# Kernel tuning notes

Measured on AMD Instinct MI355X. Metric: run time of the kernel, lower is better.

## Reference

```python
import jax, jax.numpy as jnp
import numpy as np
import math

NUM_HEADS = 16
HEAVY_RATIO = 0.1
RECENT_RATIO = 0.1
ROPE_THETA = 10000.0


def setup_inputs() -> dict:
    key = jax.random.key(0)
    ks = jax.random.split(key, 5)
    b, s, h = 1, 2048, 2048
    return {
        "hidden_states": jax.random.normal(ks[0], (b, s, h), dtype=jnp.float32),
        "Wq": jax.random.normal(ks[1], (h, h), dtype=jnp.float32) * 0.02,
        "Wk": jax.random.normal(ks[2], (h, h), dtype=jnp.float32) * 0.02,
        "Wv": jax.random.normal(ks[3], (h, h), dtype=jnp.float32) * 0.02,
        "Wo": jax.random.normal(ks[4], (h, h), dtype=jnp.float32) * 0.02,
    }


def _rotate_half(x):
    d = x.shape[-1]
    return jnp.concatenate([-x[..., d // 2:], x[..., : d // 2]], axis=-1)


def _rope(q, k, seq_len, head_dim, dtype):
    # LLaMA rotary embedding: inv_freq over even dims, emb = [freqs, freqs]
    inv_freq = 1.0 / (ROPE_THETA ** (jnp.arange(0, head_dim, 2, dtype=jnp.float32) / head_dim))
    pos = jnp.arange(seq_len, dtype=jnp.float32)
    freqs = pos[:, None] * inv_freq[None, :]            # [s, d/2]
    emb = jnp.concatenate([freqs, freqs], axis=-1)       # [s, d]
    cos = jnp.cos(emb).astype(dtype)[None, None]         # [1,1,s,d]
    sin = jnp.sin(emb).astype(dtype)[None, None]
    q = q * cos + _rotate_half(q) * sin
    k = k * cos + _rotate_half(k) * sin
    return q, k


def reference(hidden_states, Wq, Wk, Wv, Wo):
    b, s, hidden = hidden_states.shape
    H = NUM_HEADS
    d = hidden // H

    def proj(W):  # nn.Linear(x) = x @ W.T, then split heads -> [b,H,s,d]
        return (hidden_states @ W.T).reshape(b, s, H, d).transpose(0, 2, 1, 3)

    q, k, v = proj(Wq), proj(Wk), proj(Wv)
    q, k = _rope(q, k, s, d, hidden_states.dtype)

    scores = jnp.einsum("bhqd,bhkd->bhqk", q, k) / math.sqrt(d)  # [b,H,s,s]
    neg = jnp.finfo(scores.dtype).min
    i = jnp.arange(s)[:, None]
    j = jnp.arange(s)[None, :]
    causal = jnp.where(j <= i, jnp.array(0.0, scores.dtype), neg)
    scores = jnp.maximum(scores + causal, neg)

    heavy_budget = int(HEAVY_RATIO * s)
    recent_budget = int(RECENT_RATIO * s)

    # first softmax (fp32), accumulate column importances
    tmp_attn = jax.nn.softmax(scores.astype(jnp.float32), axis=-1).astype(scores.dtype)
    tmp_sum = jnp.sum(tmp_attn, axis=-2)                 # [b,H,s]
    _, topk_idx = jax.lax.top_k(tmp_sum, heavy_budget)   # [b,H,heavy]
    heavy_mask = jnp.any(topk_idx[..., :, None] == jnp.arange(s)[None, None, None, :], axis=-2)  # [b,H,s]

    # recent band: tril(diag=recent) & triu(diag=-recent)  <=>  |i-j| <= recent
    band = jnp.abs(i - j) <= recent_budget               # [s,s]
    mask = heavy_mask[:, :, None, :] | band[None, None]

    scores = jnp.where(mask, scores, neg)
    probs = jax.nn.softmax(scores.astype(jnp.float32), axis=-1).astype(q.dtype)
    attn = jnp.einsum("bhqk,bhkd->bhqd", probs, v)
    attn = attn.transpose(0, 2, 1, 3).reshape(b, s, hidden)
    return attn @ Wo.T
```

## Files before the change

### kernel.cpp

```cpp
#include <hip/hip_runtime.h>
#include <hip/hip_bf16.h>
#include <stdint.h>

#define SEQ   2048
#define HIDN  2048
#define NHEAD 16
#define HDIM  128
#define HEAVY 204
#define RECENT 204

typedef __attribute__((ext_vector_type(4))) float f32x4;
typedef __attribute__((ext_vector_type(8))) short bf16x8;
typedef unsigned short u16;
typedef unsigned int   u32;

static __device__ __forceinline__ u16 f2bf(float f){
  union { float f; u32 u; } v; v.f = f;
  u32 r = (v.u + 0x7FFFu + ((v.u >> 16) & 1u)) >> 16;
  return (u16)r;
}
static __device__ __forceinline__ float bf2f(u16 u){
  union { u32 u; float f; } v; v.u = ((u32)u) << 16;
  return v.f;
}

static __device__ __forceinline__ void gload16(const void* g, void* l){
  __builtin_amdgcn_global_load_lds((const __attribute__((address_space(1))) u32*)g,
                                   (__attribute__((address_space(3))) u32*)l, 16, 0, 0);
}

#define WAITVM(N) asm volatile("s_waitcnt vmcnt(" #N ")" ::: "memory")
#define BARRAW    __builtin_amdgcn_s_barrier()
#define PRIO1     __builtin_amdgcn_s_setprio(1)
#define PRIO0     __builtin_amdgcn_s_setprio(0)

static __device__ __forceinline__ void stage_tile(const u16* __restrict__ base, size_t stride,
                                                  int row0, u16* __restrict__ lds, int tid){
  const int wbase = tid & ~63;
#pragma unroll
  for (int it = 0; it < 4; ++it){
    int m = it * 256 + tid;
    int row = m >> 4, cp = m & 15;
    gload16(base + (size_t)(row0 + row) * stride + ((cp ^ (row & 7)) * 8),
            lds + (it * 256 + wbase) * 8);
  }
}

static __device__ __forceinline__ void stageK512(const u16* __restrict__ base, size_t stride,
                                                 int row0, u16* __restrict__ lds, int tid){
#pragma unroll
  for (int it = 0; it < 2; ++it){
    int m = it * 512 + tid;
    int row = m >> 4, cp = m & 15;
    gload16(base + (size_t)(row0 + row) * stride + ((cp ^ (row & 7)) * 8),
            lds + (it * 512 + (tid & ~63)) * 8);
  }
}
static __device__ __forceinline__ void stageV512(const u16* __restrict__ base, size_t stride,
                                                 int c0, u16* __restrict__ lds, int tid){
#pragma unroll
  for (int it = 0; it < 2; ++it){
    int m = it * 512 + tid;
    int row = m >> 3, cp = m & 7;
    gload16(base + (size_t)row * stride + c0 + ((cp ^ (row & 7)) * 8),
            lds + (it * 512 + (tid & ~63)) * 8);
  }
}

__global__ void k_prep(const float* __restrict__ A0, const float* __restrict__ A1,
                       const float* __restrict__ A2, const float* __restrict__ A3,
                       const float* __restrict__ A4, u16* __restrict__ out,
                       float* __restrict__ cosT, float* __restrict__ sinT,
                       float* __restrict__ colsum){
  int b = blockIdx.x, tid = threadIdx.x;
  if (b < 20480){
    int id = b * 256 + tid;
    int sel = id >> 20, off = (id & 1048575) * 4;
    const float* src = sel == 0 ? A0 : sel == 1 ? A1 : sel == 2 ? A2 : sel == 3 ? A3 : A4;
    float4 v = *(const float4*)(src + off);
    ushort4 o;
    o.x = f2bf(v.x); o.y = f2bf(v.y); o.z = f2bf(v.z); o.w = f2bf(v.w);
    *(ushort4*)(out + (size_t)sel * 4194304 + off) = o;
  } else if (b < 20992){
    int i = (b - 20480) * 256 + tid;
    int pos = i >> 6, j = i & 63;
    float invf = powf(10000.0f, -(float)j * (1.0f / 64.0f));
    float a = (float)pos * invf;
    cosT[i] = cosf(a);
    sinT[i] = sinf(a);
  } else {
    int i = (b - 20992) * 256 + tid;
    if (i < 16384) ((float4*)colsum)[i] = (float4){0.f, 0.f, 0.f, 0.f};
  }
}

__global__ void k_post(u16* __restrict__ Qm, u16* __restrict__ Km,
                       const float* __restrict__ cosT, const float* __restrict__ sinT,
                       const u16* __restrict__ V, u16* __restrict__ Vt){
  __shared__ u16 t[32][33];
  int b = blockIdx.x, tid = threadIdx.x;
  if (b < 4096){
    int gid = b * 256 + tid;
    u16* M = (gid < 524288) ? Qm : Km;
    int id = gid & 524287;
    int pos = id >> 8, rem = id & 255;
    int h = rem >> 4, j4 = (rem & 15) * 4;
    u16* p = M + (size_t)pos * HIDN + h * HDIM + j4;
    ushort4 lo = *(ushort4*)p;
    ushort4 hi = *(ushort4*)(p + 64);
    float4 c = *(const float4*)(cosT + pos * 64 + j4);
    float4 s = *(const float4*)(sinT + pos * 64 + j4);
    float l0 = bf2f(lo.x), l1 = bf2f(lo.y), l2 = bf2f(lo.z), l3 = bf2f(lo.w);
    float h0 = bf2f(hi.x), h1 = bf2f(hi.y), h2 = bf2f(hi.z), h3 = bf2f(hi.w);
    ushort4 nlo, nhi;
    nlo.x = f2bf(l0 * c.x - h0 * s.x);  nhi.x = f2bf(h0 * c.x + l0 * s.x);
    nlo.y = f2bf(l1 * c.y - h1 * s.y);  nhi.y = f2bf(h1 * c.y + l1 * s.y);
    nlo.z = f2bf(l2 * c.z - h2 * s.z);  nhi.z = f2bf(h2 * c.z + l2 * s.z);
    nlo.w = f2bf(l3 * c.w - h3 * s.w);  nhi.w = f2bf(h3 * c.w + l3 * s.w);
    *(ushort4*)p = nlo;
    *(ushort4*)(p + 64) = nhi;
  } else {
    int b2 = b - 4096;
    int s0 = (b2 & 63) * 32, c0 = (b2 >> 6) * 32;
    int r = tid >> 3, cc = (tid & 7) * 4;
    ushort4 v = *(const ushort4*)(V + (size_t)(s0 + r) * 2048 + c0 + cc);
    t[r][cc] = v.x; t[r][cc + 1] = v.y; t[r][cc + 2] = v.z; t[r][cc + 3] = v.w;
    __syncthreads();
    int co = tid >> 3, ro = (tid & 7) * 4;
    ushort4 o;
    o.x = t[ro][co]; o.y = t[ro + 1][co]; o.z = t[ro + 2][co]; o.w = t[ro + 3][co];
    *(ushort4*)(Vt + (size_t)(c0 + co) * 2048 + s0 + ro) = o;
  }
}

__global__ __launch_bounds__(512, 1)
void k_g256(const u16* __restrict__ X, const u16* __restrict__ Wq, const u16* __restrict__ Wk,
            const u16* __restrict__ Wv, u16* __restrict__ C0, u16* __restrict__ C1,
            u16* __restrict__ C2){
  __shared__ __align__(16) u16 LA[2][256 * 64];
  __shared__ __align__(16) u16 LB[2][192 * 64];
  const int tid = threadIdx.x;
  const int lane = tid & 63, wvi = tid >> 6;
  const int wm = wvi >> 2, wn = wvi & 3;
  const int g = lane >> 4, c15 = lane & 15;
  const int brow = blockIdx.y * 256;
  const int bcol = blockIdx.x * 192;
  const int NT = 32;

  f32x4 acc[8][3];
#pragma unroll
  for (int m = 0; m < 8; m++)
#pragma unroll
    for (int n = 0; n < 3; n++) acc[m][n] = (f32x4){0.f, 0.f, 0.f, 0.f};

  const int cc0 = ((g ^ (c15 & 7)) * 8);
  bf16x8 af[4][2], af2[4][2], bf[3][2];

#define BPTR(rB_) (rB_ < 2048 ? Wq + (size_t)(rB_) * 2048 \
                 : rB_ < 4096 ? Wk + (size_t)((rB_) - 2048) * 2048 \
                              : Wv + (size_t)((rB_) - 4096) * 2048)
#define STGA(grow0, gcol0, ldsb) do { \
  _Pragma("unroll") for (int it = 0; it < 2; ++it){ \
    int m_ = it * 512 + tid; \
    int row_ = m_ >> 3, cp_ = m_ & 7; \
    gload16(X + (size_t)((grow0) + row_) * 2048 + (gcol0) + ((cp_ ^ (row_ & 7)) * 8), \
            (ldsb) + (it * 512 + (tid & ~63)) * 8); \
  } } while(0)
#define STGB128(gcol0, ldsb) do { \
  _Pragma("unroll") for (int it = 0; it < 2; ++it){ \
    int m_ = it * 512 + tid; \
    int row_ = m_ >> 3, cp_ = m_ & 7; \
    int rB_ = bcol + row_; \
    const u16* bp_ = BPTR(rB_); \
    gload16(bp_ + (gcol0) + ((cp_ ^ (row_ & 7)) * 8), \
            (ldsb) + (it * 512 + (tid & ~63)) * 8); \
  } } while(0)
#define STGB64(gcol0, ldsb) do { \
    int row_ = 128 + (tid >> 3), cp_ = tid & 7; \
    int rB_ = bcol + row_; \
    const u16* bp_ = BPTR(rB_); \
    gload16(bp_ + (gcol0) + ((cp_ ^ (row_ & 7)) * 8), \
            (ldsb) + (tid & ~63) * 8); \
  } while(0)
#define RDA(buf) \
  _Pragma("unroll") for (int mi2 = 0; mi2 < 4; ++mi2){ \
    const u16* pr = &LA[buf][0] + (size_t)(wm * 128 + mi2 * 16 + c15) * 64; \
    af[mi2][0] = *(const bf16x8*)(pr + cc0); \
    af[mi2][1] = *(const bf16x8*)(pr + (cc0 ^ 32)); \
  }
#define RDA2(buf) \
  _Pragma("unroll") for (int mi2 = 0; mi2 < 4; ++mi2){ \
    const u16* pr = &LA[buf][0] + (size_t)(wm * 128 + (4 + mi2) * 16 + c15) * 64; \
    af2[mi2][0] = *(const bf16x8*)(pr + cc0); \
    af2[mi2][1] = *(const bf16x8*)(pr + (cc0 ^ 32)); \
  }
#define RDB2(buf) \
  _Pragma("unroll") for (int ni2 = 0; ni2 < 2; ++ni2){ \
    const u16* pr = &LB[buf][0] + (size_t)(wn * 48 + ni2 * 16 + c15) * 64; \
    bf[ni2][0] = *(const bf16x8*)(pr + cc0); \
    bf[ni2][1] = *(const bf16x8*)(pr + (cc0 ^ 32)); \
  }
#define RDB1(buf) do { \
    const u16* pr = &LB[buf][0] + (size_t)(wn * 48 + 32 + c15) * 64; \
    bf[2][0] = *(const bf16x8*)(pr + cc0); \
    bf[2][1] = *(const bf16x8*)(pr + (cc0 ^ 32)); \
  } while(0)
#define MM2A \
  _Pragma("unroll") for (int mi2 = 0; mi2 < 4; ++mi2) \
  _Pragma("unroll") for (int ni2 = 0; ni2 < 2; ++ni2) \
  _Pragma("unroll") for (int kk = 0; kk < 2; ++kk) \
    acc[mi2][ni2] = __builtin_amdgcn_mfma_f32_16x16x32_bf16( \
        af[mi2][kk], bf[ni2][kk], acc[mi2][ni2], 0, 0, 0);
#define MM1AB \
  _Pragma("unroll") for (int mi2 = 0; mi2 < 4; ++mi2) \
  _Pragma("unroll") for (int kk = 0; kk < 2; ++kk){ \
    acc[mi2][2] = __builtin_amdgcn_mfma_f32_16x16x32_bf16( \
        af[mi2][kk], bf[2][kk], acc[mi2][2], 0, 0, 0); \
    acc[4 + mi2][2] = __builtin_amdgcn_mfma_f32_16x16x32_bf16( \
        af2[mi2][kk], bf[2][kk], acc[4 + mi2][2], 0, 0, 0); \
  }
#define MM2B \
  _Pragma("unroll") for (int mi2 = 0; mi2 < 4; ++mi2) \
  _Pragma("unroll") for (int ni2 = 0; ni2 < 2; ++ni2) \
  _Pragma("unroll") for (int kk = 0; kk < 2; ++kk) \
    acc[4 + mi2][ni2] = __builtin_amdgcn_mfma_f32_16x16x32_bf16( \
        af2[mi2][kk], bf[ni2][kk], acc[4 + mi2][ni2], 0, 0, 0);

#define TILE(t, buf) do { \
    const int kn1 = ((t) + 1) * 64; \
    const int kn2 = ((t) + 2) * 64; \
    RDA(buf); RDB2(buf); RDA2(buf); RDB1(buf); \
    if ((t) + 1 < NT){ STGA(brow, kn1, &LA[buf ^ 1][0]); \
                       STGA(brow + 128, kn1, &LA[buf ^ 1][0] + 128 * 64); } \
    PRIO1; MM2A; MM1AB; PRIO0; \
    BARRAW; \
    if ((t) + 2 < NT){ STGB128(kn2, &LB[buf][0]); STGB64(kn2, &LB[buf][0] + 128 * 64); } \
    PRIO1; MM2B; PRIO0; \
    if ((t) + 2 < NT){ WAITVM(3); } \
    else if ((t) + 1 < NT){ WAITVM(0); } \
    BARRAW; \
  } while(0)

  STGA(brow,       0, &LA[0][0]);
  STGA(brow + 128, 0, &LA[0][0] + 128 * 64);
  STGB128(0,  &LB[0][0]);
  STGB64(0,   &LB[0][0] + 128 * 64);
  STGB128(64, &LB[1][0]);
  STGB64(64,  &LB[1][0] + 128 * 64);
  WAITVM(3);
  BARRAW;

  for (int t = 0; t < NT; t += 2){
    TILE(t, 0);
    TILE(t + 1, 1);
  }
#undef TILE
#undef BPTR
#undef STGA
#undef STGB128
#undef STGB64
#undef RDA
#undef RDA2
#undef RDB2
#undef RDB1
#undef MM2A
#undef MM1AB
#undef MM2B

#pragma unroll
  for (int mi = 0; mi < 8; ++mi)
#pragma unroll
    for (int ni = 0; ni < 3; ++ni){
      int colbase = bcol + wn * 48 + ni * 16;
      int proj = colbase >> 11;
      u16* Cb = proj == 0 ? C0 : proj == 1 ? C1 : C2;
      int lc = (colbase & 2047) + c15;
#pragma unroll
      for (int r = 0; r < 4; ++r){
        int row = brow + wm * 128 + mi * 16 + g * 4 + r;
        Cb[(size_t)row * 2048 + lc] = f2bf(acc[mi][ni][r]);
      }
    }
}

__global__ __launch_bounds__(512)
void k_gemm_out(const u16* __restrict__ A, const u16* __restrict__ B, float* __restrict__ C){
  __shared__ __align__(16) u16 As[2][128 * 64];
  __shared__ __align__(16) u16 Bs[2][128 * 64];
  const int tid = threadIdx.x;
  const int w = tid >> 6, lane = tid & 63;
  const int wm = w >> 1, wn = w & 1;
  const int g = lane >> 4, c15 = lane & 15;
  const int brow = blockIdx.y * 128, bcol = blockIdx.x * 128;
  const int cc0 = ((g ^ (c15 & 7)) * 8);

  f32x4 acc[2][4];
#pragma unroll
  for (int m = 0; m < 2; m++)
#pragma unroll
    for (int n = 0; n < 4; n++) acc[m][n] = (f32x4){0.f, 0.f, 0.f, 0.f};

#define STG_O(k0, buf) do { \
  _Pragma("unroll") for (int it = 0; it < 2; ++it){ \
    int m_ = it * 512 + tid; \
    int row_ = m_ >> 3, cp_ = m_ & 7; \
    gload16(A + (size_t)(brow + row_) * 2048 + (k0) + ((cp_ ^ (row_ & 7)) * 8), \
            As[buf] + (it * 512 + (tid & ~63)) * 8); \
    gload16(B + (size_t)(bcol + row_) * 2048 + (k0) + ((cp_ ^ (row_ & 7)) * 8), \
            Bs[buf] + (it * 512 + (tid & ~63)) * 8); \
  } } while(0)

  STG_O(0, 0);
  int cur = 0;
  for (int kt = 0; kt < 32; ++kt){
    if (kt + 1 < 32){ STG_O((kt + 1) * 64, cur ^ 1); WAITVM(4); }
    else            { WAITVM(0); }
    BARRAW;
    bf16x8 af[2][2], bfr[4][2];
#pragma unroll
    for (int mi = 0; mi < 2; ++mi){
      const u16* pr = As[cur] + (size_t)(wm * 32 + mi * 16 + c15) * 64;
      af[mi][0] = *(const bf16x8*)(pr + cc0);
      af[mi][1] = *(const bf16x8*)(pr + (cc0 ^ 32));
    }
#pragma unroll
    for (int ni = 0; ni < 4; ++ni){
      const u16* pr = Bs[cur] + (size_t)(wn * 64 + ni * 16 + c15) * 64;
      bfr[ni][0] = *(const bf16x8*)(pr + cc0);
      bfr[ni][1] = *(const bf16x8*)(pr + (cc0 ^ 32));
    }
    PRIO1;
#pragma unroll
    for (int mi = 0; mi < 2; ++mi)
#pragma unroll
      for (int ni = 0; ni < 4; ++ni)
#pragma unroll
        for (int kk = 0; kk < 2; ++kk)
          acc[mi][ni] = __builtin_amdgcn_mfma_f32_16x16x32_bf16(af[mi][kk], bfr[ni][kk],
                                                                acc[mi][ni], 0, 0, 0);
    PRIO0;
    BARRAW;
    cur ^= 1;
  }
#undef STG_O
#pragma unroll
  for (int mi = 0; mi < 2; ++mi)
#pragma unroll
    for (int ni = 0; ni < 4; ++ni)
#pragma unroll
      for (int r = 0; r < 4; ++r){
        int row = brow + wm * 32 + mi * 16 + g * 4 + r;
        int col = bcol + wn * 64 + ni * 16 + c15;
        C[(size_t)row * 2048 + col] = acc[mi][ni][r];
      }
}

__global__ __launch_bounds__(256)
void k_pass1a(const u16* __restrict__ Q, const u16* __restrict__ K, float* __restrict__ rowsum){
  __shared__ __align__(16) u16 Ks[3][64 * 128];
  const int tid = threadIdx.x;
  const int wv = tid >> 6, lane = tid & 63;
  const int g = lane >> 4, c15 = lane & 15;
  const int h = blockIdx.y;
  int qb = 0, c = 0;
  { int rem = blockIdx.x; int q = 0;
    while (rem >= ((2 * q + 9) >> 3)){ rem -= (2 * q + 9) >> 3; q++; }
    qb = q; c = rem; }
  const int i0 = qb * 128;
  const int ktend = 2 * qb + 2;
  const int kt0 = c * 8;
  const int kt1 = (ktend < kt0 + 8) ? ktend : (kt0 + 8);
  const u16* Qh = Q + h * HDIM;
  const u16* Kh = K + h * HDIM;
  const float scale = 0.08838834764831845f;
  const int wb = wv * 32;

  bf16x8 qfr[2][4];
#pragma unroll
  for (int m = 0; m < 2; m++)
#pragma unroll
    for (int ks = 0; ks < 4; ks++)
      qfr[m][ks] = *(const bf16x8*)(Qh + (size_t)(i0 + wb + m * 16 + c15) * 2048 + ks * 32 + g * 8);

  stage_tile(Kh, 2048, kt0 * 64, Ks[0], tid);
  if (kt0 + 1 < kt1) stage_tile(Kh, 2048, (kt0 + 1) * 64, Ks[1], tid);

  float rs[2][4] = {{0.f,0.f,0.f,0.f},{0.f,0.f,0.f,0.f}};
  for (int kt = kt0; kt < kt1; ++kt){
    const int bi = (kt - kt0) % 3;
    if (kt + 1 < kt1){ WAITVM(4); } else { WAITVM(0); }
    BARRAW;
    if (kt + 2 < kt1) stage_tile(Kh, 2048, (kt + 2) * 64, Ks[(kt - kt0 + 2) % 3], tid);
    const int k0 = kt * 64;
    f32x4 sacc[2][4];
#pragma unroll
    for (int m = 0; m < 2; m++)
#pragma unroll
      for (int n = 0; n < 4; n++) sacc[m][n] = (f32x4){0.f, 0.f, 0.f, 0.f};
#pragma unroll
    for (int ks = 0; ks < 4; ++ks){
#pragma unroll
      for (int n = 0; n < 4; n++){
        int brw = n * 16 + c15;
        bf16x8 b = *(const bf16x8*)(Ks[bi] + brw * 128 + ((ks * 32 + g * 8) ^ ((brw & 7) << 3)));
#pragma unroll
        for (int m = 0; m < 2; m++)
          sacc[m][n] = __builtin_amdgcn_mfma_f32_16x16x32_bf16(qfr[m][ks], b, sacc[m][n], 0, 0, 0);
      }
    }
    if (kt < 2 * qb){
#pragma unroll
      for (int m = 0; m < 2; m++)
#pragma unroll
        for (int n = 0; n < 4; n++)
#pragma unroll
          for (int r = 0; r < 4; r++)
            rs[m][r] += __expf(sacc[m][n][r] * scale);
    } else {
#pragma unroll
      for (int n = 0; n < 4; n++){
        int col = k0 + n * 16 + c15;
#pragma unroll
        for (int m = 0; m < 2; m++)
#pragma unroll
          for (int r = 0; r < 4; r++){
            int rowg = i0 + wb + m * 16 + g * 4 + r;
            rs[m][r] += (col <= rowg) ? __expf(sacc[m][n][r] * scale) : 0.f;
          }
      }
    }
  }
#pragma unroll
  for (int m = 0; m < 2; m++)
#pragma unroll
    for (int r = 0; r < 4; r++){
      float v = rs[m][r];
      v += __shfl_xor(v, 1); v += __shfl_xor(v, 2);
      v += __shfl_xor(v, 4); v += __shfl_xor(v, 8);
      if (c15 == 0)
        atomicAdd(&rowsum[h * 2048 + i0 + wb + m * 16 + g * 4 + r], v);
    }
}

__global__ __launch_bounds__(256)
void k_pass1b(const u16* __restrict__ Q, const u16* __restrict__ K,
              const float* __restrict__ rowsum, float* __restrict__ colsum){
  __shared__ __align__(16) u16 Qs[3][64 * 128];
  const int tid = threadIdx.x;
  const int wv = tid >> 6, lane = tid & 63;
  const int g = lane >> 4, c15 = lane & 15;
  const int h = blockIdx.y;
  int kb = 0, c = 0;
  { int rem = blockIdx.x; int q = 0;
    while (rem >= ((39 - 2 * q) >> 3)){ rem -= (39 - 2 * q) >> 3; q++; }
    kb = q; c = rem; }
  const int k0 = kb * 128;
  const int qt0 = 2 * kb + c * 8;
  const int qt1 = (2 * kb + c * 8 + 8 < 32) ? (2 * kb + c * 8 + 8) : 32;
  const u16* Qh = Q + h * HDIM;
  const u16* Kh = K + h * HDIM;
  const float scale = 0.08838834764831845f;
  const int wb = wv * 32;
  const float* rsrow = rowsum + h * 2048;

  bf16x8 kfr[2][4];
#pragma unroll
  for (int m = 0; m < 2; m++)
#pragma unroll
    for (int ks = 0; ks < 4; ks++)
      kfr[m][ks] = *(const bf16x8*)(Kh + (size_t)(k0 + wb + m * 16 + c15) * 2048 + ks * 32 + g * 8);

  stage_tile(Qh, 2048, qt0 * 64, Qs[0], tid);
  if (qt0 + 1 < qt1) stage_tile(Qh, 2048, (qt0 + 1) * 64, Qs[1], tid);

  float racc[2][4] = {{0.f,0.f,0.f,0.f},{0.f,0.f,0.f,0.f}};
  for (int qt = qt0; qt < qt1; ++qt){
    const int bi = (qt - qt0) % 3;
    if (qt + 1 < qt1){ WAITVM(4); } else { WAITVM(0); }
    BARRAW;
    if (qt + 2 < qt1) stage_tile(Qh, 2048, (qt + 2) * 64, Qs[(qt - qt0 + 2) % 3], tid);
    const int i0q = qt * 64;
    float rw[4];
#pragma unroll
    for (int n = 0; n < 4; n++)
      rw[n] = 1.0f / rsrow[i0q + n * 16 + c15];
    f32x4 sacc[2][4];
#pragma unroll
    for (int m = 0; m < 2; m++)
#pragma unroll
      for (int n = 0; n < 4; n++) sacc[m][n] = (f32x4){0.f, 0.f, 0.f, 0.f};
#pragma unroll
    for (int ks = 0; ks < 4; ++ks){
#pragma unroll
      for (int n = 0; n < 4; n++){
        int brw = n * 16 + c15;
        bf16x8 b = *(const bf16x8*)(Qs[bi] + brw * 128 + ((ks * 32 + g * 8) ^ ((brw & 7) << 3)));
#pragma unroll
        for (int m = 0; m < 2; m++)
          sacc[m][n] = __builtin_amdgcn_mfma_f32_16x16x32_bf16(kfr[m][ks], b, sacc[m][n], 0, 0, 0);
      }
    }
    if (qt >= 2 * kb + 2){
#pragma unroll
      for (int m = 0; m < 2; m++)
#pragma unroll
        for (int n = 0; n < 4; n++)
#pragma unroll
          for (int r = 0; r < 4; r++)
            racc[m][r] += __expf(sacc[m][n][r] * scale) * rw[n];
    } else {
#pragma unroll
      for (int n = 0; n < 4; n++){
        int colq = i0q + n * 16 + c15;
#pragma unroll
        for (int m = 0; m < 2; m++)
#pragma unroll
          for (int r = 0; r < 4; r++){
            int rowk = k0 + wb + m * 16 + g * 4 + r;
            racc[m][r] += (rowk <= colq) ? __expf(sacc[m][n][r] * scale) * rw[n] : 0.f;
          }
      }
    }
  }
#pragma unroll
  for (int m = 0; m < 2; m++)
#pragma unroll
    for (int r = 0; r < 4; r++){
      float v = racc[m][r];
      v += __shfl_xor(v, 1); v += __shfl_xor(v, 2);
      v += __shfl_xor(v, 4); v += __shfl_xor(v, 8);
      if (c15 == 0)
        atomicAdd(&colsum[h * 2048 + k0 + wb + m * 16 + g * 4 + r], v);
    }
}

__global__ __launch_bounds__(1024)
void k_topk(const float* __restrict__ colsum, short* __restrict__ cidx){
  __shared__ u32 keys[2048];
  __shared__ int hist[256];
  __shared__ int chunkCnt[32];
  __shared__ short cidL[256];
  __shared__ u32 Tacc_s;
  __shared__ int rem_s;
  const int tid = threadIdx.x;
  const int h = blockIdx.x;
  const int w = tid >> 6, lane = tid & 63;

  for (int i = tid; i < 2048; i += 1024) keys[i] = ((const u32*)colsum)[h * 2048 + i];
  if (tid == 0){ Tacc_s = 0; rem_s = HEAVY; }
  __syncthreads();

  for (int s = 24; s >= 0; s -= 8){
    if (tid < 256) hist[tid] = 0;
    __syncthreads();
    u32 T = Tacc_s;
    for (int i = tid; i < 2048; i += 1024){
      u32 k = keys[i];
      bool match = (s == 24) ? true : (((k ^ T) >> (s + 8)) == 0);
      if (match) atomicAdd(&hist[(k >> s) & 255], 1);
    }
    __syncthreads();
    if (tid == 0){
      int rem = rem_s, acc = 0, b = 255;
      for (; b > 0; --b){
        int c2 = hist[b];
        if (acc + c2 >= rem) break;
        acc += c2;
      }
      Tacc_s = T | ((u32)b << s);
      rem_s = rem - acc;
    }
    __syncthreads();
  }
  const u32 T = Tacc_s;
  const int need = rem_s;
  const u32 kA = keys[tid], kB = keys[tid + 1024];
  const bool eqA = (kA == T), eqB = (kB == T);
  unsigned long long ebA = __ballot(eqA);
  unsigned long long ebB = __ballot(eqB);
  if (lane == 0){ chunkCnt[w] = __popcll(ebA); chunkCnt[16 + w] = __popcll(ebB); }
  __syncthreads();
  if (tid == 0){
    int s2 = 0;
    for (int i2 = 0; i2 < 32; ++i2){ int c2 = chunkCnt[i2]; chunkCnt[i2] = s2; s2 += c2; }
  }
  __syncthreads();
  const unsigned long long below = (1ull << lane) - 1ull;
  const int eqrA = chunkCnt[w] + __popcll(ebA & below);
  const int eqrB = chunkCnt[16 + w] + __popcll(ebB & below);
  const bool hvA = (kA > T) || (eqA && eqrA < need);
  const bool hvB = (kB > T) || (eqB && eqrB < need);
  __syncthreads();
  unsigned long long hbA = __ballot(hvA);
  unsigned long long hbB = __ballot(hvB);
  if (lane == 0){ chunkCnt[w] = __popcll(hbA); chunkCnt[16 + w] = __popcll(hbB); }
  if (tid >= HEAVY && tid < 256) cidL[tid] = 32767;
  __syncthreads();
  if (tid == 0){
    int s2 = 0;
    for (int i2 = 0; i2 < 32; ++i2){ int c2 = chunkCnt[i2]; chunkCnt[i2] = s2; s2 += c2; }
  }
  __syncthreads();
  if (hvA) cidL[chunkCnt[w] + __popcll(hbA & below)] = (short)tid;
  if (hvB) cidL[chunkCnt[16 + w] + __popcll(hbB & below)] = (short)(tid + 1024);
  __syncthreads();
  if (tid < 256) cidx[h * 256 + tid] = cidL[tid];
}

__global__ void k_gath(const u16* __restrict__ Kb, const u16* __restrict__ Vb,
                       const short* __restrict__ cidx,
                       u16* __restrict__ Kg, u16* __restrict__ Vg){
  __shared__ __align__(16) u16 t[32][136];
  int b = blockIdx.x, tid = threadIdx.x;
  if (b < 256){
    int gid = b * 256 + tid;
    int h = gid >> 12, rem = gid & 4095;
    int slot = rem >> 4, cp = rem & 15;
    int cid = cidx[h * 256 + slot];
    bf16x8 z = (bf16x8){0,0,0,0,0,0,0,0};
    bf16x8 val = (cid < 2048) ? *(const bf16x8*)(Kb + (size_t)cid * 2048 + h * 128 + cp * 8) : z;
    *(bf16x8*)(Kg + ((size_t)h * 256 + slot) * 128 + cp * 8) = val;
  } else {
    int b2 = b - 256;
    int h = b2 >> 3, s0 = (b2 & 7) * 32;
#pragma unroll
    for (int it = 0; it < 2; ++it){
      int m = it * 256 + tid;
      int s = m >> 4, cp = m & 15;
      int cid = cidx[h * 256 + s0 + s];
      bf16x8 z = (bf16x8){0,0,0,0,0,0,0,0};
      bf16x8 val = (cid < 2048) ? *(const bf16x8*)(Vb + (size_t)cid * 2048 + h * 128 + cp * 8) : z;
      *(bf16x8*)(&t[s][cp * 8]) = val;
    }
    __syncthreads();
#pragma unroll
    for (int i = 0; i < 16; ++i){
      int idx = i * 256 + tid;
      int d = idx >> 5, s = idx & 31;
      Vg[((size_t)h * 128 + d) * 256 + s0 + s] = t[s][d];
    }
  }
}

__global__ __launch_bounds__(512)
void k_pass2(const u16* __restrict__ Q, const u16* __restrict__ K, const u16* __restrict__ Vt,
             const u16* __restrict__ Kg, const u16* __restrict__ Vg,
             const short* __restrict__ cidx, u16* __restrict__ attn){
  __shared__ __align__(16) u16 Ks[2][64 * 128];
  __shared__ __align__(16) u16 Vs[2][128 * 64];
  __shared__ __align__(16) u16 Ps[8][16 * 64];
  __shared__ short cids[256];
  __shared__ int lists[12];
  __shared__ int nact_s;
  const int tid = threadIdx.x;
  const int w = tid >> 6, lane = tid & 63;
  const int g = lane >> 4, c15 = lane & 15;
  const int qb = blockIdx.x, h = blockIdx.y;
  const int i0 = qb * 128;
  const int wq = w >> 2, w4 = w & 3;
  const int rowbase = i0 + wq * 64 + w4 * 16;
  const u16* Qh = Q + h * HDIM;
  const u16* Kh = K + h * HDIM;
  const u16* Kgh = Kg + (size_t)h * 256 * 128;
  const u16* Vth = Vt + (size_t)h * 128 * 2048;
  const u16* Vgh = Vg + (size_t)h * 128 * 256;
  const float scale = 0.08838834764831845f;

  if (tid < 256) cids[tid] = cidx[h * 256 + tid];
  bf16x8 qfr[4];
#pragma unroll
  for (int ks = 0; ks < 4; ks++)
    qfr[ks] = *(const bf16x8*)(Qh + (size_t)(rowbase + c15) * 2048 + ks * 32 + g * 8);
  __syncthreads();
  if (tid == 0){
    int n = 0;
    int ktb0 = (i0 > RECENT) ? ((i0 - RECENT) >> 6) : 0;
    int ktmax = (i0 + 127) >> 6;
    for (int kt = ktb0; kt <= ktmax; ++kt) lists[n++] = kt;
    for (int gt = 0; gt < 4; ++gt)
      if ((int)cids[gt * 64] <= i0 + 127 - RECENT - 1) lists[n++] = 100 + gt;
    nact_s = n;
  }
  __syncthreads();
  const int nact = nact_s;

  { int e = lists[0];
    if (e < 100){ stageK512(Kh, 2048, e * 64, Ks[0], tid);
                  stageV512(Vth, 2048, e * 64, Vs[0], tid); }
    else        { stageK512(Kgh, 128, (e - 100) * 64, Ks[0], tid);
                  stageV512(Vgh, 256, (e - 100) * 64, Vs[0], tid); } }

  f32x4 oacc[8];
#pragma unroll
  for (int f = 0; f < 8; f++) oacc[f] = (f32x4){0.f, 0.f, 0.f, 0.f};
  float lsum[4] = {0.f, 0.f, 0.f, 0.f};

  int cur = 0;
  for (int i = 0; i < nact; ++i){
    const int e = lists[i];
    const bool isg = (e >= 100);
    const bool nxt = (i + 1 < nact);
    WAITVM(2);
    BARRAW;
    if (nxt){
      int e2 = lists[i + 1];
      if (e2 < 100){ stageK512(Kh, 2048, e2 * 64, Ks[cur ^ 1], tid);
                     stageV512(Vth, 2048, e2 * 64, Vs[cur ^ 1], tid); }
      else         { stageK512(Kgh, 128, (e2 - 100) * 64, Ks[cur ^ 1], tid);
                     stageV512(Vgh, 256, (e2 - 100) * 64, Vs[cur ^ 1], tid); }
    }
    f32x4 sacc[4];
#pragma unroll
    for (int n = 0; n < 4; n++) sacc[n] = (f32x4){0.f, 0.f, 0.f, 0.f};
#pragma unroll
    for (int ks = 0; ks < 4; ++ks){
#pragma unroll
      for (int n = 0; n < 4; n++){
        int brw = n * 16 + c15;
        bf16x8 b = *(const bf16x8*)(Ks[cur] + brw * 128 + ((ks * 32 + g * 8) ^ ((brw & 7) << 3)));
        sacc[n] = __builtin_amdgcn_mfma_f32_16x16x32_bf16(qfr[ks], b, sacc[n], 0, 0, 0);
      }
    }
#pragma unroll
    for (int n = 0; n < 4; n++){
      int cid = isg ? (int)cids[(e - 100) * 64 + n * 16 + c15] : (e * 64 + n * 16 + c15);
#pragma unroll
      for (int r = 0; r < 4; r++){
        int rowg = rowbase + g * 4 + r;
        int dist = rowg - cid;
        bool valid = (cid <= rowg) && (isg ? (dist > RECENT) : (dist <= RECENT));
        float ev = valid ? __expf(sacc[n][r] * scale) : 0.f;
        lsum[r] += ev;
        int prow = g * 4 + r;
        Ps[w][prow * 64 + ((n * 16 + c15) ^ ((prow & 7) << 3))] = f2bf(ev);
      }
    }
    if (nxt) WAITVM(4); else WAITVM(0);
    BARRAW;
    PRIO1;
#pragma unroll
    for (int ks2 = 0; ks2 < 2; ++ks2){
      bf16x8 pa = *(const bf16x8*)(&Ps[w][c15 * 64 + ((ks2 * 32 + g * 8) ^ ((c15 & 7) << 3))]);
#pragma unroll
      for (int f = 0; f < 8; ++f){
        int vrow = f * 16 + c15;
        bf16x8 vb = *(const bf16x8*)(Vs[cur] + vrow * 64 + ((ks2 * 32 + g * 8) ^ ((vrow & 7) << 3)));
        oacc[f] = __builtin_amdgcn_mfma_f32_16x16x32_bf16(pa, vb, oacc[f], 0, 0, 0);
      }
    }
    PRIO0;
    cur ^= 1;
  }
  float rinv[4];
#pragma unroll
  for (int r = 0; r < 4; r++){
    float v = lsum[r];
    v += __shfl_xor(v, 1); v += __shfl_xor(v, 2);
    v += __shfl_xor(v, 4); v += __shfl_xor(v, 8);
    rinv[r] = 1.0f / v;
  }
#pragma unroll
  for (int f = 0; f < 8; f++)
#pragma unroll
    for (int r = 0; r < 4; r++){
      int rowg = rowbase + g * 4 + r;
      attn[(size_t)rowg * 2048 + h * HDIM + f * 16 + c15] = f2bf(oacc[f][r] * rinv[r]);
    }
}

extern "C" void kernel_launch(void* const* d_in, const int* in_sizes, int n_in,
                              void* d_out, int out_size, void* d_ws, size_t ws_size,
                              hipStream_t stream){
  const float* X  = (const float*)d_in[0];
  const float* Wq = (const float*)d_in[1];
  const float* Wk = (const float*)d_in[2];
  const float* Wv = (const float*)d_in[3];
  const float* Wo = (const float*)d_in[4];

  char* w = (char*)d_ws;
  const size_t MB8 = (size_t)2048 * 2048 * 2;
  u16* Xb  = (u16*)(w);
  u16* Wqb = (u16*)(w + 1 * MB8);
  u16* Wkb = (u16*)(w + 2 * MB8);
  u16* Wvb = (u16*)(w + 3 * MB8);
  u16* Wob = (u16*)(w + 4 * MB8);
  u16* Qb  = (u16*)(w + 5 * MB8);
  u16* Kb  = (u16*)(w + 6 * MB8);
  u16* Vb  = (u16*)(w + 7 * MB8);
  u16* Vtb   = Wqb;
  u16* attnb = Xb;
  char* p = w + 8 * MB8;
  float* cosT = (float*)p;              p += 524288;
  float* sinT = (float*)p;              p += 524288;
  float* colsum = (float*)p;            p += 131072;
  float* rowsum = (float*)p;            p += 131072;
  short* cidx  = (short*)p;             p += 16 * 256 * 2;
  u16*   Kg    = (u16*)p;               p += (size_t)16 * 256 * 128 * 2;
  u16*   Vg    = (u16*)p;

  dim3 b256(256);

  k_prep<<<21056, b256, 0, stream>>>(X, Wq, Wk, Wv, Wo, Xb, cosT, sinT, colsum);

  k_g256<<<dim3(32, 8), dim3(512), 0, stream>>>(Xb, Wqb, Wkb, Wvb, Qb, Kb, Vb);
  k_post<<<8192, b256, 0, stream>>>(Qb, Kb, cosT, sinT, Vb, Vtb);

  k_pass1a<<<dim3(40, 16), b256, 0, stream>>>(Qb, Kb, rowsum);
  k_pass1b<<<dim3(40, 16), b256, 0, stream>>>(Qb, Kb, rowsum, colsum);
  k_topk<<<16, dim3(1024), 0, stream>>>(colsum, cidx);
  k_gath<<<384, b256, 0, stream>>>(Kb, Vb, cidx, Kg, Vg);
  k_pass2<<<dim3(16, 16), dim3(512), 0, stream>>>(Qb, Kb, Vtb, Kg, Vg, cidx, attnb);

  k_gemm_out<<<dim3(16, 16), dim3(512), 0, stream>>>(attnb, Wob, (float*)d_out);
}
```

Before: 239.1 us.

## Shrink QKV GEMM tiles to 128x192x32 for higher occupancy

Restructures the fused QKV projection GEMM from 256x192 tiles with K-step 64 and a hand-interleaved split-phase pipeline into 128x192 tiles with K-step 32 and a simple double-buffered loop. The grid doubles to 512 blocks, and launch bounds allow up to 4 blocks per CU. The aim is better CU fill and latency hiding on a 256-CU device, where 256 blocks leave each CU with a single block. In exchange, each block reuses data less, A/B loads and barriers per FLOP rise, and the finely interleaved MFMA/load schedule is lost.

Result: slower. 252.4 us (+5.6%).

```diff
diff --git a/kernel.cpp b/kernel.cpp
--- a/kernel.cpp
+++ b/kernel.cpp
@@ -133,142 +133,72 @@
   }
 }
 
-__global__ __launch_bounds__(512, 1)
+__global__ __launch_bounds__(512, 4)
 void k_g256(const u16* __restrict__ X, const u16* __restrict__ Wq, const u16* __restrict__ Wk,
             const u16* __restrict__ Wv, u16* __restrict__ C0, u16* __restrict__ C1,
             u16* __restrict__ C2){
-  __shared__ __align__(16) u16 LA[2][256 * 64];
-  __shared__ __align__(16) u16 LB[2][192 * 64];
+  __shared__ __align__(16) u16 LA[2][128 * 32];
+  __shared__ __align__(16) u16 LB[2][192 * 32];
   const int tid = threadIdx.x;
   const int lane = tid & 63, wvi = tid >> 6;
   const int wm = wvi >> 2, wn = wvi & 3;
   const int g = lane >> 4, c15 = lane & 15;
-  const int brow = blockIdx.y * 256;
+  const int brow = blockIdx.y * 128;
   const int bcol = blockIdx.x * 192;
-  const int NT = 32;
-
-  f32x4 acc[8][3];
-#pragma unroll
-  for (int m = 0; m < 8; m++)
+  const int NT = 64;
+  const int cc = (g ^ (c15 & 3)) * 8;
+
+  f32x4 acc[4][3];
+#pragma unroll
+  for (int m = 0; m < 4; m++)
 #pragma unroll
     for (int n = 0; n < 3; n++) acc[m][n] = (f32x4){0.f, 0.f, 0.f, 0.f};
-
-  const int cc0 = ((g ^ (c15 & 7)) * 8);
-  bf16x8 af[4][2], af2[4][2], bf[3][2];
 
 #define BPTR(rB_) (rB_ < 2048 ? Wq + (size_t)(rB_) * 2048 \
                  : rB_ < 4096 ? Wk + (size_t)((rB_) - 2048) * 2048 \
                               : Wv + (size_t)((rB_) - 4096) * 2048)
-#define STGA(grow0, gcol0, ldsb) do { \
-  _Pragma("unroll") for (int it = 0; it < 2; ++it){ \
-    int m_ = it * 512 + tid; \
-    int row_ = m_ >> 3, cp_ = m_ & 7; \
-    gload16(X + (size_t)((grow0) + row_) * 2048 + (gcol0) + ((cp_ ^ (row_ & 7)) * 8), \
-            (ldsb) + (it * 512 + (tid & ~63)) * 8); \
-  } } while(0)
-#define STGB128(gcol0, ldsb) do { \
-  _Pragma("unroll") for (int it = 0; it < 2; ++it){ \
-    int m_ = it * 512 + tid; \
-    int row_ = m_ >> 3, cp_ = m_ & 7; \
-    int rB_ = bcol + row_; \
-    const u16* bp_ = BPTR(rB_); \
-    gload16(bp_ + (gcol0) + ((cp_ ^ (row_ & 7)) * 8), \
-            (ldsb) + (it * 512 + (tid & ~63)) * 8); \
-  } } while(0)
-#define STGB64(gcol0, ldsb) do { \
-    int row_ = 128 + (tid >> 3), cp_ = tid & 7; \
-    int rB_ = bcol + row_; \
-    const u16* bp_ = BPTR(rB_); \
-    gload16(bp_ + (gcol0) + ((cp_ ^ (row_ & 7)) * 8), \
-            (ldsb) + (tid & ~63) * 8); \
+#define STG(kt, buf) do { \
+    const int k0_ = (kt) * 32; \
+    { int row_ = tid >> 2, cp_ = tid & 3; \
+      gload16(X + (size_t)(brow + row_) * 2048 + k0_ + ((cp_ ^ (row_ & 3)) * 8), \
+              &LA[buf][0] + (tid & ~63) * 8); } \
+    { int row_ = tid >> 2, cp_ = tid & 3; int rB_ = bcol + row_; \
+      const u16* bp_ = BPTR(rB_); \
+      gload16(bp_ + k0_ + ((cp_ ^ (row_ & 3)) * 8), \
+              &LB[buf][0] + (tid & ~63) * 8); } \
+    { int c2_ = 512 + (tid & 255); int row_ = c2_ >> 2, cp_ = c2_ & 3; int rB_ = bcol + row_; \
+      const u16* bp_ = BPTR(rB_); \
+      gload16(bp_ + k0_ + ((cp_ ^ (row_ & 3)) * 8), \
+              &LB[buf][0] + (512 + (tid & 192)) * 8); } \
   } while(0)
-#define RDA(buf) \
-  _Pragma("unroll") for (int mi2 = 0; mi2 < 4; ++mi2){ \
-    const u16* pr = &LA[buf][0] + (size_t)(wm * 128 + mi2 * 16 + c15) * 64; \
-    af[mi2][0] = *(const bf16x8*)(pr + cc0); \
-    af[mi2][1] = *(const bf16x8*)(pr + (cc0 ^ 32)); \
-  }
-#define RDA2(buf) \
-  _Pragma("unroll") for (int mi2 = 0; mi2 < 4; ++mi2){ \
-    const u16* pr = &LA[buf][0] + (size_t)(wm * 128 + (4 + mi2) * 16 + c15) * 64; \
-    af2[mi2][0] = *(const bf16x8*)(pr + cc0); \
-    af2[mi2][1] = *(const bf16x8*)(pr + (cc0 ^ 32)); \
-  }
-#define RDB2(buf) \
-  _Pragma("unroll") for (int ni2 = 0; ni2 < 2; ++ni2){ \
-    const u16* pr = &LB[buf][0] + (size_t)(wn * 48 + ni2 * 16 + c15) * 64; \
-    bf[ni2][0] = *(const bf16x8*)(pr + cc0); \
-    bf[ni2][1] = *(const bf16x8*)(pr + (cc0 ^ 32)); \
-  }
-#define RDB1(buf) do { \
-    const u16* pr = &LB[buf][0] + (size_t)(wn * 48 + 32 + c15) * 64; \
-    bf[2][0] = *(const bf16x8*)(pr + cc0); \
-    bf[2][1] = *(const bf16x8*)(pr + (cc0 ^ 32)); \
-  } while(0)
-#define MM2A \
-  _Pragma("unroll") for (int mi2 = 0; mi2 < 4; ++mi2) \
-  _Pragma("unroll") for (int ni2 = 0; ni2 < 2; ++ni2) \
-  _Pragma("unroll") for (int kk = 0; kk < 2; ++kk) \
-    acc[mi2][ni2] = __builtin_amdgcn_mfma_f32_16x16x32_bf16( \
-        af[mi2][kk], bf[ni2][kk], acc[mi2][ni2], 0, 0, 0);
-#define MM1AB \
-  _Pragma("unroll") for (int mi2 = 0; mi2 < 4; ++mi2) \
-  _Pragma("unroll") for (int kk = 0; kk < 2; ++kk){ \
-    acc[mi2][2] = __builtin_amdgcn_mfma_f32_16x16x32_bf16( \
-        af[mi2][kk], bf[2][kk], acc[mi2][2], 0, 0, 0); \
-    acc[4 + mi2][2] = __builtin_amdgcn_mfma_f32_16x16x32_bf16( \
-        af2[mi2][kk], bf[2][kk], acc[4 + mi2][2], 0, 0, 0); \
-  }
-#define MM2B \
-  _Pragma("unroll") for (int mi2 = 0; mi2 < 4; ++mi2) \
-  _Pragma("unroll") for (int ni2 = 0; ni2 < 2; ++ni2) \
-  _Pragma("unroll") for (int kk = 0; kk < 2; ++kk) \
-    acc[4 + mi2][ni2] = __builtin_amdgcn_mfma_f32_16x16x32_bf16( \
-        af2[mi2][kk], bf[ni2][kk], acc[4 + mi2][ni2], 0, 0, 0);
-
-#define TILE(t, buf) do { \
-    const int kn1 = ((t) + 1) * 64; \
-    const int kn2 = ((t) + 2) * 64; \
-    RDA(buf); RDB2(buf); RDA2(buf); RDB1(buf); \
-    if ((t) + 1 < NT){ STGA(brow, kn1, &LA[buf ^ 1][0]); \
-                       STGA(brow + 128, kn1, &LA[buf ^ 1][0] + 128 * 64); } \
-    PRIO1; MM2A; MM1AB; PRIO0; \
-    BARRAW; \
-    if ((t) + 2 < NT){ STGB128(kn2, &LB[buf][0]); STGB64(kn2, &LB[buf][0] + 128 * 64); } \
-    PRIO1; MM2B; PRIO0; \
-    if ((t) + 2 < NT){ WAITVM(3); } \
-    else if ((t) + 1 < NT){ WAITVM(0); } \
-    BARRAW; \
-  } while(0)
-
-  STGA(brow,       0, &LA[0][0]);
-  STGA(brow + 128, 0, &LA[0][0] + 128 * 64);
-  STGB128(0,  &LB[0][0]);
-  STGB64(0,   &LB[0][0] + 128 * 64);
-  STGB128(64, &LB[1][0]);
-  STGB64(64,  &LB[1][0] + 128 * 64);
-  WAITVM(3);
-  BARRAW;
-
-  for (int t = 0; t < NT; t += 2){
-    TILE(t, 0);
-    TILE(t + 1, 1);
-  }
-#undef TILE
+
+  STG(0, 0);
+  for (int t = 0; t < NT; ++t){
+    const int buf = t & 1;
+    if (t + 1 < NT){ STG(t + 1, buf ^ 1); WAITVM(3); }
+    else           { WAITVM(0); }
+    BARRAW;
+    bf16x8 af[4], bfv[3];
+#pragma unroll
+    for (int mi = 0; mi < 4; ++mi)
+      af[mi] = *(const bf16x8*)(&LA[buf][0] + (size_t)(wm * 64 + mi * 16 + c15) * 32 + cc);
+#pragma unroll
+    for (int ni = 0; ni < 3; ++ni)
+      bfv[ni] = *(const bf16x8*)(&LB[buf][0] + (size_t)(wn * 48 + ni * 16 + c15) * 32 + cc);
+    PRIO1;
+#pragma unroll
+    for (int mi = 0; mi < 4; ++mi)
+#pragma unroll
+      for (int ni = 0; ni < 3; ++ni)
+        acc[mi][ni] = __builtin_amdgcn_mfma_f32_16x16x32_bf16(af[mi], bfv[ni], acc[mi][ni], 0, 0, 0);
+    PRIO0;
+    BARRAW;
+  }
+#undef STG
 #undef BPTR
-#undef STGA
-#undef STGB128
-#undef STGB64
-#undef RDA
-#undef RDA2
-#undef RDB2
-#undef RDB1
-#undef MM2A
-#undef MM1AB
-#undef MM2B
-
-#pragma unroll
-  for (int mi = 0; mi < 8; ++mi)
+
+#pragma unroll
+  for (int mi = 0; mi < 4; ++mi)
 #pragma unroll
     for (int ni = 0; ni < 3; ++ni){
       int colbase = bcol + wn * 48 + ni * 16;
@@ -277,7 +207,7 @@
       int lc = (colbase & 2047) + c15;
 #pragma unroll
       for (int r = 0; r < 4; ++r){
-        int row = brow + wm * 128 + mi * 16 + g * 4 + r;
+        int row = brow + wm * 64 + mi * 16 + g * 4 + r;
         Cb[(size_t)row * 2048 + lc] = f2bf(acc[mi][ni][r]);
       }
     }
@@ -802,7 +732,7 @@
 
   k_prep<<<21056, b256, 0, stream>>>(X, Wq, Wk, Wv, Wo, Xb, cosT, sinT, colsum);
 
-  k_g256<<<dim3(32, 8), dim3(512), 0, stream>>>(Xb, Wqb, Wkb, Wvb, Qb, Kb, Vb);
+  k_g256<<<dim3(32, 16), dim3(512), 0, stream>>>(Xb, Wqb, Wkb, Wvb, Qb, Kb, Vb);
   k_post<<<8192, b256, 0, stream>>>(Qb, Kb, cosT, sinT, Vb, Vtb);
 
   k_pass1a<<<dim3(40, 16), b256, 0, stream>>>(Qb, Kb, rowsum);
```
